# Optimization experiments

Measured on AMD Instinct MI355X. Metric: run time of the kernel, lower is better.

The kernel has to match this reference:

```python
import jax, jax.numpy as jnp
import numpy as np

N, M, DIST, HEADS, D, C, DFFN = 16384, 16, 2, 8, 256, 64, 512
DH = D // HEADS
GRID = 128
BLOCK = 2048  # mirrors torch batch_size loop in find_neighboring_voxels_optimized
EPS = 1e-5


def _neighbors(coords_f, src, m, dist):
    """Blockwise Manhattan-distance topk neighbor gather.
    coords_f: (N,3) float voxel coords; src: (N,D) features.
    Returns (N, m, D) neighbor features, zero-filled where fewer than m in range."""
    n = coords_f.shape[0]
    qblocks = coords_f.reshape(-1, BLOCK, 3)

    def one_block(cb):
        # (BLOCK, N) Manhattan distances
        d = jnp.abs(cb[:, None, :] - coords_f[None, :, :]).sum(-1)
        d = jnp.where(d <= dist, d, jnp.inf)
        vals, idx = jax.lax.top_k(-d, m)          # nearest m (self first: dist 0)
        valid = (vals > -jnp.inf)[..., None]
        return jnp.where(valid, src[idx], jnp.zeros((), src.dtype))

    return jax.lax.map(one_block, qblocks).reshape(n, m, src.shape[-1])


def _layernorm(x, g, b):
    mu = x.mean(-1, keepdims=True)
    var = ((x - mu) ** 2).mean(-1, keepdims=True)
    return (x - mu) * jax.lax.rsqrt(var + EPS) * g + b


def setup_inputs() -> dict:
    key = jax.random.key(0)
    ks = jax.random.split(key, 32)
    p = lambda i, shape, s: jax.random.normal(ks[i], shape, dtype=jnp.float32) * s
    z = lambda shape: jnp.zeros(shape, dtype=jnp.float32)
    o = lambda shape: jnp.ones(shape, dtype=jnp.float32)
    return {
        "coords": jax.random.randint(ks[0], (N, 3), 0, GRID, dtype=jnp.int32),
        "features": jax.random.normal(ks[1], (N, C), dtype=jnp.float32),
        "pe_w1": p(2, (3, D // 2), 0.5), "pe_b1": z((D // 2,)),
        "pe_w2": p(3, (D // 2, D), 0.08), "pe_b2": z((D,)),
        "proj_w": p(4, (C, D), 0.12), "proj_b": z((D,)),
        "wq": p(5, (D, D), 0.06), "bq": z((D,)),
        "wk": p(6, (D, D), 0.06), "bk": z((D,)),
        "wv": p(7, (D, D), 0.06), "bv": z((D,)),
        "wo": p(8, (D, D), 0.06), "bo": z((D,)),
        "ffn_w1": p(9, (D, DFFN), 0.06), "ffn_b1": z((DFFN,)),
        "ffn_w2": p(10, (DFFN, D), 0.04), "ffn_b2": z((D,)),
        "ln_g": o((D,)), "ln_b": z((D,)),
        "fus_w1": p(11, (D, C), 0.06), "fus_b1": z((C,)),
        "fus_w2": p(12, (2 * C, C), 0.09), "fus_b2": z((C,)),
        "bn_g": o((C,)), "bn_b": z((C,)),
    }


def reference(coords, features, pe_w1, pe_b1, pe_w2, pe_b2, proj_w, proj_b,
              wq, bq, wk, bk, wv, bv, wo, bo,
              ffn_w1, ffn_b1, ffn_w2, ffn_b2, ln_g, ln_b,
              fus_w1, fus_b1, fus_w2, fus_b2, bn_g, bn_b):
    coords_f = coords.astype(jnp.float32)
    # dynamic learnable positional encoding on normalized coords
    xn = coords_f / (GRID - 1)
    pe = jax.nn.relu(xn @ pe_w1 + pe_b1) @ pe_w2 + pe_b2
    src = features @ proj_w + proj_b + pe                       # (N, D)

    nf = _neighbors(coords_f, src, M, DIST)                     # (N, M, D)
    query = nf[:, 0, :]                                         # (N, D) self-feature

    # multihead attention: query len 1, key len M, batch N
    q = (query @ wq + bq).reshape(N, HEADS, DH)
    k = (nf @ wk + bk).reshape(N, M, HEADS, DH)
    v = (nf @ wv + bv).reshape(N, M, HEADS, DH)
    scores = jnp.einsum('nhd,nmhd->nhm', q, k) / jnp.sqrt(jnp.float32(DH))
    attn = jax.nn.softmax(scores, axis=-1)
    ao = jnp.einsum('nhm,nmhd->nhd', attn, v).reshape(N, D) @ wo + bo  # (N, D)

    # FFN with residual + LayerNorm (dropout=0 / eval)
    h = jax.nn.relu(ao @ ffn_w1 + ffn_b1) @ ffn_w2 + ffn_b2
    y = _layernorm(ao + h, ln_g, ln_b)                          # (N, D)

    # EnhancedFusion: project, concat, linear, BatchNorm1d (batch stats), ReLU
    t = y @ fus_w1 + fus_b1                                     # (N, C)
    f = jnp.concatenate([features, t], axis=1) @ fus_w2 + fus_b2
    mu = f.mean(0)
    var = ((f - mu) ** 2).mean(0)
    f = (f - mu) * jax.lax.rsqrt(var + EPS) * bn_g + bn_b
    return jax.nn.relu(f)                                       # (N, C)
```

## Files before the change

kernel.cpp:

```cpp
#include <hip/hip_runtime.h>
#include <stdint.h>

typedef unsigned short u16;
typedef unsigned int   u32;
typedef __attribute__((ext_vector_type(8))) short short8;
typedef __attribute__((ext_vector_type(4))) float f32x4;

static constexpr int kN = 16384;
static constexpr float kEPS = 1e-5f;

__device__ __forceinline__ u16 f2bf(float x) {
  u32 u = __float_as_uint(x);
  u32 r = (u + 0x7fffu + ((u >> 16) & 1u)) >> 16;
  return (u16)r;
}
__device__ __forceinline__ float bf2f(u16 x) {
  return __uint_as_float(((u32)x) << 16);
}
__device__ __forceinline__ void ldbf8(const u16* p, float* o) {
  uint4 v = *(const uint4*)p;
  o[0] = __uint_as_float(v.x << 16);  o[1] = __uint_as_float(v.x & 0xffff0000u);
  o[2] = __uint_as_float(v.y << 16);  o[3] = __uint_as_float(v.y & 0xffff0000u);
  o[4] = __uint_as_float(v.z << 16);  o[5] = __uint_as_float(v.z & 0xffff0000u);
  o[6] = __uint_as_float(v.w << 16);  o[7] = __uint_as_float(v.w & 0xffff0000u);
}
__device__ __forceinline__ void gll16(const u16* g, u16* l) {
  __builtin_amdgcn_global_load_lds(
      (const __attribute__((address_space(1))) void*)g,
      (__attribute__((address_space(3))) void*)l, 16, 0, 0);
}

struct WSet {
  const float* s[6]; u16* d[6];
  int K[6]; int N[6]; int dstride[6]; int coff[6];
};

__global__ __launch_bounds__(256) void k_setup(WSet ws,
                                               u32* __restrict__ zero_area,
                                               const float* __restrict__ proj_b,
                                               const float* __restrict__ pe_b2,
                                               const float* __restrict__ uw1,
                                               const float* __restrict__ ub1,
                                               const float* __restrict__ uw2,
                                               const float* __restrict__ ub2,
                                               u16* __restrict__ W2f,
                                               float* __restrict__ bbf,
                                               const int* __restrict__ coords,
                                               const float* __restrict__ feats,
                                               const float* __restrict__ pw1,
                                               const float* __restrict__ pb1,
                                               u16* __restrict__ A1,
                                               u16* __restrict__ A2,
                                               const float* __restrict__ wq,
                                               const float* __restrict__ wk,
                                               const float* __restrict__ wv,
                                               const float* __restrict__ proj_w_f,
                                               const float* __restrict__ pe_w2_f,
                                               u16* __restrict__ W1K,
                                               float* __restrict__ bcomb) {
  int w = blockIdx.y;
  if (w == 6) {
    int idx = blockIdx.x * 256 + threadIdx.x;
    if (idx < 33088) zero_area[idx] = 0u;
    return;
  }
  if (w == 7) {
    int n = blockIdx.x;
    if (n >= 64) return;
    int k = threadIdx.x;
    float s = 0.f;
    for (int j = 0; j < 64; j++) s += uw1[k * 64 + j] * uw2[(64 + j) * 64 + n];
    W2f[n * 320 + k] = f2bf(s);
    if (k < 64) W2f[n * 320 + 256 + k] = f2bf(uw2[k * 64 + n]);
    if (k == 0) {
      float b = ub2[n];
      for (int j = 0; j < 64; j++) b += ub1[j] * uw2[(64 + j) * 64 + n];
      bbf[n] = b;
    }
    return;
  }
  if (w == 8) {
    int r0 = blockIdx.x * 32;
#pragma unroll
    for (int s = 0; s < 3; s++) {
      int j = threadIdx.x + s * 256;
      int row = j / 24, seg = j % 24;
      int n = r0 + row;
      u16 o[8];
      if (seg < 8) {
        const float* fp = feats + (size_t)n * 64 + seg * 8;
        float4 a = *(const float4*)fp;
        float4 b = *(const float4*)(fp + 4);
        o[0] = f2bf(a.x); o[1] = f2bf(a.y); o[2] = f2bf(a.z); o[3] = f2bf(a.w);
        o[4] = f2bf(b.x); o[5] = f2bf(b.y); o[6] = f2bf(b.z); o[7] = f2bf(b.w);
        *(uint4*)(A2 + (size_t)n * 320 + 256 + seg * 8) = *(uint4*)o;
      } else {
        int jj0 = (seg - 8) * 8;
        float x0 = (float)coords[n * 3 + 0] * (1.f / 127.f);
        float x1 = (float)coords[n * 3 + 1] * (1.f / 127.f);
        float x2 = (float)coords[n * 3 + 2] * (1.f / 127.f);
#pragma unroll
        for (int u = 0; u < 8; u++) {
          int jj = jj0 + u;
          float hv = pb1[jj] + x0 * pw1[jj] + x1 * pw1[128 + jj] + x2 * pw1[256 + jj];
          o[u] = f2bf(fmaxf(hv, 0.f));
        }
      }
      *(uint4*)(A1 + (size_t)n * 192 + seg * 8) = *(uint4*)o;
    }
    return;
  }
  if (w == 9) {
    int bx = blockIdx.x;
    if (bx < 3) {
      const float* wsel = (bx == 0) ? wq : (bx == 1) ? wk : wv;
      int c = threadIdx.x;
      float s = 0.f;
      for (int d = 0; d < 256; d++) s += (proj_b[d] + pe_b2[d]) * wsel[d * 256 + c];
      bcomb[bx * 256 + c] = s;
    } else if (bx < 27) {
      int i0 = (bx - 3) * 2048 + threadIdx.x * 8;
      const float* src = (i0 < 16384) ? (proj_w_f + i0) : (pe_w2_f + (i0 - 16384));
      float4 a = *(const float4*)src;
      float4 b = *(const float4*)(src + 4);
      u16 o[8];
      o[0] = f2bf(a.x); o[1] = f2bf(a.y); o[2] = f2bf(a.z); o[3] = f2bf(a.w);
      o[4] = f2bf(b.x); o[5] = f2bf(b.y); o[6] = f2bf(b.z); o[7] = f2bf(b.w);
      *(uint4*)(W1K + i0) = *(uint4*)o;
    }
    return;
  }
  const float* S = ws.s[w]; u16* D = ws.d[w];
  int K = ws.K[w], N = ws.N[w], ds = ws.dstride[w], co = ws.coff[w];
  int ntx = N >> 5, tiles = ntx * (K >> 5);
  int t = blockIdx.x;
  if (t >= tiles) return;
  int n0 = (t % ntx) * 32, k0 = (t / ntx) * 32;
  __shared__ float st[32][33];
  int tr = threadIdx.x >> 3, tc4 = (threadIdx.x & 7) * 4;
  float4 v = *(const float4*)(S + (size_t)(k0 + tr) * N + n0 + tc4);
  st[tc4 + 0][tr] = v.x; st[tc4 + 1][tr] = v.y;
  st[tc4 + 2][tr] = v.z; st[tc4 + 3][tr] = v.w;
  __syncthreads();
  u16 o4[4];
  o4[0] = f2bf(st[tr][tc4 + 0]); o4[1] = f2bf(st[tr][tc4 + 1]);
  o4[2] = f2bf(st[tr][tc4 + 2]); o4[3] = f2bf(st[tr][tc4 + 3]);
  *(uint2*)(D + (size_t)(n0 + tr) * ds + co + k0 + tc4) = *(uint2*)o4;
}


__global__ __launch_bounds__(256) void k_hist(const int* __restrict__ coords,
                                              u32* __restrict__ cnt) {
  int n = blockIdx.x * 256 + threadIdx.x;
  int c = coords[n * 3] * 128 + coords[n * 3 + 1];
  atomicAdd(&cnt[c], 1u);
}

__global__ __launch_bounds__(256) void k_scan(const u32* __restrict__ cnt,
                                              u32* __restrict__ startb) {
  __shared__ u32 tots[256];
  int t = threadIdx.x;
  int base = t * 64;
  u32 s = 0;
  for (int i = 0; i < 64; i++) s += cnt[base + i];
  tots[t] = s;
  __syncthreads();
  if (t == 0) {
    u32 run = 0;
    for (int i = 0; i < 256; i++) { u32 v = tots[i]; tots[i] = run; run += v; }
  }
  __syncthreads();
  u32 run = tots[t];
  for (int i = 0; i < 64; i++) { startb[base + i] = run; run += cnt[base + i]; }
}

__global__ __launch_bounds__(256) void k_scatter(const int* __restrict__ coords,
                                                 const u32* __restrict__ startb,
                                                 u32* __restrict__ cursor,
                                                 u32* __restrict__ pts) {
  int n = blockIdx.x * 256 + threadIdx.x;
  int x = coords[n * 3], y = coords[n * 3 + 1], z = coords[n * 3 + 2];
  int c = x * 128 + y;
  u32 slot = atomicAdd(&cursor[c], 1u);
  pts[startb[c] + slot] = ((u32)z << 14) | (u32)n;
}

__global__ __launch_bounds__(256) void k_select(const int* __restrict__ coords,
                                                const u32* __restrict__ startb,
                                                const u32* __restrict__ cnt,
                                                const u32* __restrict__ pts,
                                                int* __restrict__ idxo) {
  int gid = blockIdx.x * 256 + threadIdx.x;
  u32 pk = pts[gid];
  int n = (int)(pk & 16383u);
  int z = (int)(pk >> 14);
  int x = coords[n * 3], y = coords[n * 3 + 1];
  u32 best[16];
#pragma unroll
  for (int j = 0; j < 16; j++) best[j] = 0xFFFFFFFFu;
  const int dxs[13] = {0, -1, 1, 0, 0, -2, 2, 0, 0, -1, -1, 1, 1};
  const int dys[13] = {0, 0, 0, -1, 1, 0, 0, -2, 2, -1, 1, -1, 1};
  const int dbs[13] = {0, 1, 1, 1, 1, 2, 2, 2, 2, 2, 2, 2, 2};
#pragma unroll
  for (int t = 0; t < 13; t++) {
    int xx = x + dxs[t], yy = y + dys[t];
    if (xx < 0 || xx > 127 || yy < 0 || yy > 127) continue;
    int c = xx * 128 + yy;
    u32 s0 = startb[c], e0 = s0 + cnt[c];
    for (u32 i = s0; i < e0; ++i) {
      u32 p = pts[i];
      int zq = (int)(p >> 14);
      int id = (int)(p & 16383u);
      int az = z - zq; az = az < 0 ? -az : az;
      int dd = dbs[t] + az;
      u32 key = (dd <= 2) ? (((u32)dd << 14) | (u32)id) : 0xFFFFFFFFu;
#pragma unroll
      for (int j = 0; j < 16; j++) {
        u32 lo = min(best[j], key);
        u32 hi = max(best[j], key);
        best[j] = lo; key = hi;
      }
    }
  }
#pragma unroll
  for (int j = 0; j < 16; j++)
    idxo[gid * 16 + j] = (best[j] == 0xFFFFFFFFu) ? -1 : (int)(best[j] & 16383u);
}

template <int BM, int BN, int ACT>
__global__ __launch_bounds__(256) void k_mgemm(
    const u16* __restrict__ A, const u16* __restrict__ WT,
    const float* __restrict__ bias,
    u16* __restrict__ Cout,
    int M, int K, int N) {
  constexpr int FM = BM / 32, FN = BN / 32;
  constexpr int RA = BM / 64, RB = BN / 64;
  constexpr int BNP = BN + 8;
  constexpr int STAGE = (BM + BN) * 128;
  constexpr int TILEB = BM * BNP * 2;
  constexpr int SMEMB = STAGE > TILEB ? STAGE : TILEB;
  __shared__ __align__(16) char smem[SMEMB];
  u16* AsB = (u16*)smem;
  u16* BsB = AsB + 2 * BM * 32;
  u16* tile = (u16*)smem;
  const int tid = threadIdx.x;
  const int wave = tid >> 6, lane = tid & 63;
  const int bm = blockIdx.y * BM, bn = blockIdx.x * BN;
  const int wr = (wave >> 1) * (BM / 2), wc = (wave & 1) * (BN / 2);
  const int fr = lane & 15, fk = (lane >> 4) * 8, rq = (lane >> 4) * 4;

  f32x4 acc[FM][FN];
#pragma unroll
  for (int i = 0; i < FM; i++)
#pragma unroll
    for (int j = 0; j < FN; j++)
#pragma unroll
      for (int r = 0; r < 4; r++) acc[i][j][r] = 0.f;

  for (int k0 = 0; k0 < K; k0 += 64) {
#pragma unroll
    for (int h = 0; h < 2; h++) {
#pragma unroll
      for (int r = 0; r < RA; r++) {
        int g2 = r * 256 + tid;
        gll16(A + (size_t)(bm + (g2 >> 2)) * K + k0 + h * 32 + (g2 & 3) * 8,
              AsB + h * BM * 32 + g2 * 8);
      }
#pragma unroll
      for (int r = 0; r < RB; r++) {
        int g2 = r * 256 + tid;
        gll16(WT + (size_t)(bn + (g2 >> 2)) * K + k0 + h * 32 + (g2 & 3) * 8,
              BsB + h * BN * 32 + g2 * 8);
      }
    }
    __syncthreads();
#pragma unroll
    for (int h = 0; h < 2; h++) {
      short8 af[FM], bg[FN];
#pragma unroll
      for (int i = 0; i < FM; i++)
        af[i] = *(const short8*)&AsB[h * BM * 32 + (wr + i * 16 + fr) * 32 + fk];
#pragma unroll
      for (int j = 0; j < FN; j++)
        bg[j] = *(const short8*)&BsB[h * BN * 32 + (wc + j * 16 + fr) * 32 + fk];
#pragma unroll
      for (int i = 0; i < FM; i++)
#pragma unroll
        for (int j = 0; j < FN; j++)
          acc[i][j] = __builtin_amdgcn_mfma_f32_16x16x32_bf16(af[i], bg[j], acc[i][j], 0, 0, 0);
    }
    __syncthreads();
  }

#pragma unroll
  for (int j = 0; j < FN; j++) {
    int ccl = wc + j * 16 + fr;
    float bval = bias ? bias[bn + ccl] : 0.f;
#pragma unroll
    for (int i = 0; i < FM; i++) {
      int rl = wr + i * 16 + rq;
#pragma unroll
      for (int r = 0; r < 4; r++) {
        float v = acc[i][j][r] + bval;
        if (ACT) v = fmaxf(v, 0.f);
        tile[(rl + r) * BNP + ccl] = f2bf(v);
      }
    }
  }
  __syncthreads();
  constexpr int RPW = BN / 8;
  constexpr int PT = BM * BN / 8 / 256;
#pragma unroll
  for (int t = 0; t < PT; t++) {
    int idx = t * 256 + tid;
    int row = idx / RPW, c8 = (idx % RPW) * 8;
    *(uint4*)(Cout + (size_t)(bm + row) * N + bn + c8) =
        *(const uint4*)&tile[row * BNP + c8];
  }
}

__global__ __launch_bounds__(256) void k_attn(const u16* __restrict__ QKV,
                                              const u32* __restrict__ pts,
                                              const int* __restrict__ idx,
                                              const float* __restrict__ bq,
                                              const float* __restrict__ bk,
                                              const float* __restrict__ bv,
                                              u16* __restrict__ outp) {
  int gid = blockIdx.x * 256 + threadIdx.x;
  int s4 = gid >> 3;
  int n = (int)(pts[s4] & 16383u), h = gid & 7;
  const int* ip = idx + s4 * 16;
  const int hb = h * 32;
  float q[32];
  {
    int i0 = ip[0];
    const u16* qp = QKV + (size_t)i0 * 768 + hb;
#pragma unroll
    for (int j = 0; j < 32; j += 8) ldbf8(qp + j, &q[j]);
#pragma unroll
    for (int j = 0; j < 32; j++) q[j] += bq[hb + j];
  }
  float qbk = 0.f;
#pragma unroll
  for (int j = 0; j < 32; j++) qbk += q[j] * bk[hb + j];
  float s[16]; int ii[16];
#pragma unroll
  for (int m = 0; m < 16; m++) {
    int i = ip[m]; ii[m] = i;
    float d = qbk;
    if (i >= 0) {
      const u16* kp = QKV + (size_t)i * 768 + 256 + hb;
      float kv[32];
#pragma unroll
      for (int j = 0; j < 32; j += 8) ldbf8(kp + j, &kv[j]);
#pragma unroll
      for (int j = 0; j < 32; j++) d += q[j] * kv[j];
    }
    s[m] = d * 0.17677669529663689f;
  }
  float mx = s[0];
#pragma unroll
  for (int m = 1; m < 16; m++) mx = fmaxf(mx, s[m]);
  float sum = 0.f;
#pragma unroll
  for (int m = 0; m < 16; m++) { s[m] = __expf(s[m] - mx); sum += s[m]; }
  float inv = 1.f / sum;
  float o[32];
#pragma unroll
  for (int j = 0; j < 32; j++) o[j] = 0.f;
#pragma unroll
  for (int m = 0; m < 16; m++) {
    if (ii[m] >= 0) {
      const u16* vp = QKV + (size_t)ii[m] * 768 + 512 + hb;
      float vv[32];
#pragma unroll
      for (int j = 0; j < 32; j += 8) ldbf8(vp + j, &vv[j]);
#pragma unroll
      for (int j = 0; j < 32; j++) o[j] += s[m] * vv[j];
    }
  }
  u16* op = outp + (size_t)n * 256 + hb;
#pragma unroll
  for (int j = 0; j < 32; j += 8) {
    u16 tmp[8];
#pragma unroll
    for (int jj = 0; jj < 8; jj++) tmp[jj] = f2bf(o[j + jj] * inv + bv[hb + j + jj]);
    *(uint4*)(op + j) = *(uint4*)tmp;
  }
}

__global__ __launch_bounds__(256) void k_ffn2ln(const u16* __restrict__ A,
                                                const u16* __restrict__ WT,
                                                const float* __restrict__ bias,
                                                const u16* __restrict__ Addp,
                                                const float* __restrict__ g,
                                                const float* __restrict__ b,
                                                u16* __restrict__ A2) {
  constexpr int BM = 64, BN = 256, FM = 2, FN = 8;
  constexpr int ADP = 264;
  __shared__ __align__(16) char smem[(BM + BN) * 128];
  __shared__ float lnS[64][2], lnQ[64][2];
  u16* AsB = (u16*)smem;
  u16* BsB = AsB + 2 * BM * 32;
  u16* addT = (u16*)smem;
  u16* outT = (u16*)smem;
  const int tid = threadIdx.x;
  const int wave = tid >> 6, lane = tid & 63;
  const int bm = blockIdx.x * BM;
  const int wr = (wave >> 1) * 32, wc = (wave & 1) * 128;
  const int fr = lane & 15, fk = (lane >> 4) * 8, rq = (lane >> 4) * 4;

  f32x4 acc[FM][FN];
#pragma unroll
  for (int i = 0; i < FM; i++)
#pragma unroll
    for (int j = 0; j < FN; j++)
#pragma unroll
      for (int r = 0; r < 4; r++) acc[i][j][r] = 0.f;

  for (int k0 = 0; k0 < 512; k0 += 64) {
#pragma unroll
    for (int h = 0; h < 2; h++) {
      {
        int g2 = tid;
        gll16(A + (size_t)(bm + (g2 >> 2)) * 512 + k0 + h * 32 + (g2 & 3) * 8,
              AsB + h * BM * 32 + g2 * 8);
      }
#pragma unroll
      for (int r = 0; r < 4; r++) {
        int g2 = r * 256 + tid;
        gll16(WT + (size_t)(g2 >> 2) * 512 + k0 + h * 32 + (g2 & 3) * 8,
              BsB + h * BN * 32 + g2 * 8);
      }
    }
    __syncthreads();
#pragma unroll
    for (int h = 0; h < 2; h++) {
      short8 af[FM], bg[FN];
#pragma unroll
      for (int i = 0; i < FM; i++)
        af[i] = *(const short8*)&AsB[h * BM * 32 + (wr + i * 16 + fr) * 32 + fk];
#pragma unroll
      for (int j = 0; j < FN; j++)
        bg[j] = *(const short8*)&BsB[h * BN * 32 + (wc + j * 16 + fr) * 32 + fk];
#pragma unroll
      for (int i = 0; i < FM; i++)
#pragma unroll
        for (int j = 0; j < FN; j++)
          acc[i][j] = __builtin_amdgcn_mfma_f32_16x16x32_bf16(af[i], bg[j], acc[i][j], 0, 0, 0);
    }
    __syncthreads();
  }

#pragma unroll
  for (int t = 0; t < 8; t++) {
    int idx = t * 256 + tid;
    int row = idx >> 5, c8 = (idx & 31) * 8;
    *(uint4*)&addT[row * ADP + c8] =
        *(const uint4*)(Addp + (size_t)(bm + row) * 256 + c8);
  }
  __syncthreads();
#pragma unroll
  for (int j = 0; j < FN; j++) {
    int cc = wc + j * 16 + fr;
    float bval = bias[cc];
#pragma unroll
    for (int i = 0; i < FM; i++) {
      int rl = wr + i * 16 + rq;
#pragma unroll
      for (int r = 0; r < 4; r++)
        acc[i][j][r] += bval + bf2f(addT[(rl + r) * ADP + cc]);
    }
  }
#pragma unroll
  for (int i = 0; i < FM; i++) {
#pragma unroll
    for (int r = 0; r < 4; r++) {
      float sm = 0.f, sq = 0.f;
#pragma unroll
      for (int j = 0; j < FN; j++) { float t = acc[i][j][r]; sm += t; sq += t * t; }
#pragma unroll
      for (int off = 1; off < 16; off <<= 1) {
        sm += __shfl_xor(sm, off);
        sq += __shfl_xor(sq, off);
      }
      if (fr == 0) {
        int row = wr + i * 16 + rq + r;
        lnS[row][wave & 1] = sm;
        lnQ[row][wave & 1] = sq;
      }
    }
  }
  __syncthreads();
#pragma unroll
  for (int i = 0; i < FM; i++) {
#pragma unroll
    for (int r = 0; r < 4; r++) {
      int row = wr + i * 16 + rq + r;
      float sm = lnS[row][0] + lnS[row][1];
      float sq = lnQ[row][0] + lnQ[row][1];
      float mu = sm * (1.f / 256.f);
      float var = sq * (1.f / 256.f) - mu * mu;
      float rstd = rsqrtf(var + kEPS);
#pragma unroll
      for (int j = 0; j < FN; j++) {
        int cc = wc + j * 16 + fr;
        float val = (acc[i][j][r] - mu) * rstd * g[cc] + b[cc];
        outT[row * ADP + cc] = f2bf(val);
      }
    }
  }
  __syncthreads();
#pragma unroll
  for (int t = 0; t < 8; t++) {
    int idx = t * 256 + tid;
    int row = idx >> 5, c8 = (idx & 31) * 8;
    *(uint4*)(A2 + (size_t)(bm + row) * 320 + c8) =
        *(const uint4*)&outT[row * ADP + c8];
  }
}

__global__ __launch_bounds__(256) void k_fgemm(const u16* __restrict__ A2,
                                               const u16* __restrict__ W2f,
                                               const float* __restrict__ bbf,
                                               float* __restrict__ fB,
                                               float* __restrict__ pS,
                                               float* __restrict__ pQ) {
  __shared__ __align__(16) u16 As[2][2048];
  __shared__ __align__(16) u16 Bs[2][2048];
  __shared__ float colS[64][2], colQ[64][2];
  const int tid = threadIdx.x;
  const int wave = tid >> 6, lane = tid & 63;
  const int bm = blockIdx.x * 64;
  const int wr = (wave >> 1) * 32, wc = (wave & 1) * 32;
  const int fr = lane & 15, fk = (lane >> 4) * 8, rq = (lane >> 4) * 4;
  const int g = wave * 64 + lane;
  const int grow = g >> 2, gko = (g & 3) * 8;

  f32x4 acc[2][2];
#pragma unroll
  for (int i = 0; i < 2; i++)
#pragma unroll
    for (int j = 0; j < 2; j++)
#pragma unroll
      for (int r = 0; r < 4; r++) acc[i][j][r] = 0.f;
  for (int k0 = 0; k0 < 320; k0 += 64) {
#pragma unroll
    for (int h = 0; h < 2; h++) {
      gll16(A2 + (size_t)(bm + grow) * 320 + k0 + h * 32 + gko, As[h] + g * 8);
      gll16(W2f + (size_t)grow * 320 + k0 + h * 32 + gko, Bs[h] + g * 8);
    }
    __syncthreads();
#pragma unroll
    for (int h = 0; h < 2; h++) {
      short8 af[2], bg[2];
#pragma unroll
      for (int i = 0; i < 2; i++)
        af[i] = *(const short8*)&As[h][(wr + i * 16 + fr) * 32 + fk];
#pragma unroll
      for (int j = 0; j < 2; j++)
        bg[j] = *(const short8*)&Bs[h][(wc + j * 16 + fr) * 32 + fk];
#pragma unroll
      for (int i = 0; i < 2; i++)
#pragma unroll
        for (int j = 0; j < 2; j++)
          acc[i][j] = __builtin_amdgcn_mfma_f32_16x16x32_bf16(af[i], bg[j], acc[i][j], 0, 0, 0);
    }
    __syncthreads();
  }
  float cS[2] = {0.f, 0.f}, cQ[2] = {0.f, 0.f};
#pragma unroll
  for (int j = 0; j < 2; j++) {
    int col = wc + j * 16 + fr;
    float bv = bbf[col];
#pragma unroll
    for (int i = 0; i < 2; i++) {
      int rbase = bm + wr + i * 16 + rq;
#pragma unroll
      for (int r = 0; r < 4; r++) {
        float v = acc[i][j][r] + bv;
        fB[(size_t)(rbase + r) * 64 + col] = v;
        cS[j] += v; cQ[j] += v * v;
      }
    }
  }
#pragma unroll
  for (int off = 16; off < 64; off <<= 1) {
#pragma unroll
    for (int j = 0; j < 2; j++) {
      cS[j] += __shfl_xor(cS[j], off);
      cQ[j] += __shfl_xor(cQ[j], off);
    }
  }
  if ((lane >> 4) == 0) {
#pragma unroll
    for (int j = 0; j < 2; j++) {
      colS[wc + j * 16 + fr][wave >> 1] = cS[j];
      colQ[wc + j * 16 + fr][wave >> 1] = cQ[j];
    }
  }
  __syncthreads();
  if (tid < 64) {
    atomicAdd(&pS[tid], colS[tid][0] + colS[tid][1]);
    atomicAdd(&pQ[tid], colQ[tid][0] + colQ[tid][1]);
  }
}

__global__ __launch_bounds__(256) void k_bnapply(const float* __restrict__ f,
                                                 const float* __restrict__ pS,
                                                 const float* __restrict__ pQ,
                                                 const float* __restrict__ g,
                                                 const float* __restrict__ b,
                                                 float* __restrict__ out) {
  __shared__ float cf_s[64], sh_s[64];
  if (threadIdx.x < 64) {
    int c = threadIdx.x;
    float S = pS[c], Q = pQ[c];
    float m = S * (1.f / 16384.f);
    float var = Q * (1.f / 16384.f) - m * m;
    float cf = rsqrtf(var + kEPS) * g[c];
    cf_s[c] = cf;
    sh_s[c] = b[c] - m * cf;
  }
  __syncthreads();
  int gid = blockIdx.x * 256 + threadIdx.x;
  int e = gid * 4, col = e & 63;
  float4 v = *(const float4*)(f + e);
  float4 cf = *(const float4*)(cf_s + col);
  float4 sh = *(const float4*)(sh_s + col);
  float4 o;
  o.x = fmaxf(v.x * cf.x + sh.x, 0.f);
  o.y = fmaxf(v.y * cf.y + sh.y, 0.f);
  o.z = fmaxf(v.z * cf.z + sh.z, 0.f);
  o.w = fmaxf(v.w * cf.w + sh.w, 0.f);
  *(float4*)(out + e) = o;
}

extern "C" void kernel_launch(void* const* d_in, const int* in_sizes, int n_in,
                              void* d_out, int out_size, void* d_ws, size_t ws_size,
                              hipStream_t stream) {
  (void)in_sizes; (void)n_in; (void)out_size; (void)ws_size;
  const int*   coords = (const int*)d_in[0];
  const float* feats  = (const float*)d_in[1];
  const float* pe_w1  = (const float*)d_in[2];
  const float* pe_b1  = (const float*)d_in[3];
  const float* pe_w2  = (const float*)d_in[4];
  const float* pe_b2  = (const float*)d_in[5];
  const float* proj_w = (const float*)d_in[6];
  const float* proj_b = (const float*)d_in[7];
  const float* wq  = (const float*)d_in[8];
  const float* bq  = (const float*)d_in[9];
  const float* wk  = (const float*)d_in[10];
  const float* bk  = (const float*)d_in[11];
  const float* wv  = (const float*)d_in[12];
  const float* bv  = (const float*)d_in[13];
  const float* wo  = (const float*)d_in[14];
  const float* bo  = (const float*)d_in[15];
  const float* fw1 = (const float*)d_in[16];
  const float* fb1 = (const float*)d_in[17];
  const float* fw2 = (const float*)d_in[18];
  const float* fb2 = (const float*)d_in[19];
  const float* lng = (const float*)d_in[20];
  const float* lnb = (const float*)d_in[21];
  const float* uw1 = (const float*)d_in[22];
  const float* ub1 = (const float*)d_in[23];
  const float* uw2 = (const float*)d_in[24];
  const float* ub2 = (const float*)d_in[25];
  const float* bng = (const float*)d_in[26];
  const float* bnb = (const float*)d_in[27];
  float* out = (float*)d_out;

  char* Wc = (char*)d_ws;
  const size_t MB = 1u << 20;
  u16*   A1    = (u16*)(Wc + 0 * MB);
  u16*   QKVb  = (u16*)(Wc + 14 * MB);
  u16*   aoInB = (u16*)(Wc + 38 * MB);
  u16*   aoB   = (u16*)(Wc + 46 * MB);
  u16*   h1B   = (u16*)(Wc + 54 * MB);
  u16*   A2    = (u16*)(Wc + 78 * MB);
  float* fB    = (float*)(Wc + 0 * MB);

  u16* qkvT  = (u16*)(Wc + 88 * MB);
  u16* woT   = qkvT + 196608;
  u16* fw1T  = woT + 65536;
  u16* fw2T  = fw1T + 131072;
  u16* W1K   = fw2T + 131072;
  u16* W2f   = W1K + 49152;
  u16* Wcomb = W2f + 20480;
  float* bbf   = (float*)(Wcomb + 147456);
  float* bcomb = bbf + 64;

  u32* Z      = (u32*)(Wc + 90 * MB);
  u32* cnt    = Z;
  u32* cursor = Z + 16384;
  float* pS   = (float*)(Z + 32768);
  float* pQ   = (float*)(Z + 32832);
  u32* startb = Z + 33280;
  u32* pts    = Z + 49664;
  int* idxb   = (int*)(Z + 66048);

  WSet ws;
  ws.s[0] = wq;     ws.d[0] = qkvT;          ws.K[0] = 256; ws.N[0] = 256; ws.dstride[0] = 256; ws.coff[0] = 0;
  ws.s[1] = wk;     ws.d[1] = qkvT + 65536;  ws.K[1] = 256; ws.N[1] = 256; ws.dstride[1] = 256; ws.coff[1] = 0;
  ws.s[2] = wv;     ws.d[2] = qkvT + 131072; ws.K[2] = 256; ws.N[2] = 256; ws.dstride[2] = 256; ws.coff[2] = 0;
  ws.s[3] = wo;     ws.d[3] = woT;           ws.K[3] = 256; ws.N[3] = 256; ws.dstride[3] = 256; ws.coff[3] = 0;
  ws.s[4] = fw1;    ws.d[4] = fw1T;          ws.K[4] = 256; ws.N[4] = 512; ws.dstride[4] = 256; ws.coff[4] = 0;
  ws.s[5] = fw2;    ws.d[5] = fw2T;          ws.K[5] = 512; ws.N[5] = 256; ws.dstride[5] = 512; ws.coff[5] = 0;

  k_setup<<<dim3(512, 10), 256, 0, stream>>>(ws, Z, proj_b, pe_b2,
                                             uw1, ub1, uw2, ub2, W2f, bbf,
                                             coords, feats, pe_w1, pe_b1, A1, A2,
                                             wq, wk, wv, proj_w, pe_w2, W1K, bcomb);
  k_mgemm<64, 64, 0><<<dim3(3, 12), 256, 0, stream>>>(
      qkvT, W1K, nullptr, Wcomb, 768, 256, 192);
  k_hist<<<64, 256, 0, stream>>>(coords, cnt);
  k_scan<<<1, 256, 0, stream>>>(cnt, startb);
  k_scatter<<<64, 256, 0, stream>>>(coords, startb, cursor, pts);
  k_select<<<64, 256, 0, stream>>>(coords, startb, cnt, pts, idxb);
  k_mgemm<128, 128, 0><<<dim3(6, 128), 256, 0, stream>>>(
      A1, Wcomb, bcomb, QKVb, kN, 192, 768);
  k_attn<<<512, 256, 0, stream>>>(QKVb, pts, idxb, bq, bk, bv, aoInB);
  k_mgemm<128, 64, 0><<<dim3(4, 128), 256, 0, stream>>>(
      aoInB, woT, bo, aoB, kN, 256, 256);
  k_mgemm<128, 128, 1><<<dim3(4, 128), 256, 0, stream>>>(
      aoB, fw1T, fb1, h1B, kN, 256, 512);
  k_ffn2ln<<<256, 256, 0, stream>>>(h1B, fw2T, fb2, aoB, lng, lnb, A2);
  k_fgemm<<<256, 256, 0, stream>>>(A2, W2f, bbf, fB, pS, pQ);
  k_bnapply<<<1024, 256, 0, stream>>>(fB, pS, pQ, bng, bnb, out);
}
```

Before: 242.9 us.

## Fold output projection into FFN weights and merge weight-prep with histogram

Removes the separate attention output projection GEMM. Wo is folded algebraically into FFN W1 (Wcomb2 = Wo·W1, with a combined bias). The residual ao + h is computed inside the final GEMM by concatenating the attention input and h1 along K (768) against a stacked [Wo; W2] weight, so the ao tensor is never written or re-read. The small weight-combining GEMMs and the coordinate histogram are merged into one launch, and the scan now uses wave shuffles. The combined weights add extra bf16 rounding, and the last GEMM does more K work per tile.

```diff
diff --git a/kernel.cpp b/kernel.cpp
--- a/kernel.cpp
+++ b/kernel.cpp
@@ -57,7 +57,13 @@
                                                const float* __restrict__ proj_w_f,
                                                const float* __restrict__ pe_w2_f,
                                                u16* __restrict__ W1K,
-                                               float* __restrict__ bcomb) {
+                                               float* __restrict__ bcomb,
+                                               const float* __restrict__ wo_f,
+                                               const float* __restrict__ fw1_f,
+                                               const float* __restrict__ bo_f,
+                                               const float* __restrict__ fb1_f,
+                                               u16* __restrict__ woK,
+                                               float* __restrict__ bcomb2) {
   int w = blockIdx.y;
   if (w == 6) {
     int idx = blockIdx.x * 256 + threadIdx.x;
@@ -127,6 +133,19 @@
       o[0] = f2bf(a.x); o[1] = f2bf(a.y); o[2] = f2bf(a.z); o[3] = f2bf(a.w);
       o[4] = f2bf(b.x); o[5] = f2bf(b.y); o[6] = f2bf(b.z); o[7] = f2bf(b.w);
       *(uint4*)(W1K + i0) = *(uint4*)o;
+    } else if (bx < 59) {
+      int i0 = (bx - 27) * 2048 + threadIdx.x * 8;
+      float4 a = *(const float4*)(wo_f + i0);
+      float4 b = *(const float4*)(wo_f + i0 + 4);
+      u16 o[8];
+      o[0] = f2bf(a.x); o[1] = f2bf(a.y); o[2] = f2bf(a.z); o[3] = f2bf(a.w);
+      o[4] = f2bf(b.x); o[5] = f2bf(b.y); o[6] = f2bf(b.z); o[7] = f2bf(b.w);
+      *(uint4*)(woK + i0) = *(uint4*)o;
+    } else if (bx < 61) {
+      int n2 = (bx - 59) * 256 + threadIdx.x;
+      float s = fb1_f[n2];
+      for (int d = 0; d < 256; d++) s += bo_f[d] * fw1_f[d * 512 + n2];
+      bcomb2[n2] = s;
     }
     return;
   }
@@ -148,29 +167,111 @@
   *(uint2*)(D + (size_t)(n0 + tr) * ds + co + k0 + tc4) = *(uint2*)o4;
 }
 
-
-__global__ __launch_bounds__(256) void k_hist(const int* __restrict__ coords,
-                                              u32* __restrict__ cnt) {
-  int n = blockIdx.x * 256 + threadIdx.x;
-  int c = coords[n * 3] * 128 + coords[n * 3 + 1];
-  atomicAdd(&cnt[c], 1u);
-}
+__global__ __launch_bounds__(256) void k_combo(const u16* __restrict__ qkvT,
+                                               const u16* __restrict__ W1K,
+                                               u16* __restrict__ Wcomb,
+                                               const u16* __restrict__ fw1T,
+                                               const u16* __restrict__ woK,
+                                               u16* __restrict__ Wcomb2,
+                                               const int* __restrict__ coords,
+                                               u32* __restrict__ cnt) {
+  int y = blockIdx.y;
+  if (y >= 20) {
+    int n = ((y - 20) * 4 + blockIdx.x) * 256 + threadIdx.x;
+    int c = coords[n * 3] * 128 + coords[n * 3 + 1];
+    atomicAdd(&cnt[c], 1u);
+    return;
+  }
+  const u16 *A, *WT; u16* C; int K, N, bm, bn;
+  if (y < 12) {
+    if (blockIdx.x >= 3) return;
+    A = qkvT; WT = W1K; C = Wcomb; K = 256; N = 192;
+    bm = y * 64; bn = blockIdx.x * 64;
+  } else {
+    A = fw1T; WT = woK; C = Wcomb2; K = 256; N = 256;
+    bm = (y - 12) * 64; bn = blockIdx.x * 64;
+  }
+  __shared__ __align__(16) char smem[16384];
+  u16* AsB = (u16*)smem;
+  u16* BsB = AsB + 2 * 64 * 32;
+  u16* tile = (u16*)smem;
+  const int tid = threadIdx.x;
+  const int wave = tid >> 6, lane = tid & 63;
+  const int wr = (wave >> 1) * 32, wc = (wave & 1) * 32;
+  const int fr = lane & 15, fk = (lane >> 4) * 8, rq = (lane >> 4) * 4;
+  const int grow = tid >> 2, gko = (tid & 3) * 8;
+
+  f32x4 acc[2][2];
+#pragma unroll
+  for (int i = 0; i < 2; i++)
+#pragma unroll
+    for (int j = 0; j < 2; j++)
+#pragma unroll
+      for (int r = 0; r < 4; r++) acc[i][j][r] = 0.f;
+
+  for (int k0 = 0; k0 < K; k0 += 64) {
+#pragma unroll
+    for (int h = 0; h < 2; h++) {
+      gll16(A + (size_t)(bm + grow) * K + k0 + h * 32 + gko, AsB + h * 2048 + tid * 8);
+      gll16(WT + (size_t)(bn + grow) * K + k0 + h * 32 + gko, BsB + h * 2048 + tid * 8);
+    }
+    __syncthreads();
+#pragma unroll
+    for (int h = 0; h < 2; h++) {
+      short8 af[2], bg[2];
+#pragma unroll
+      for (int i = 0; i < 2; i++)
+        af[i] = *(const short8*)&AsB[h * 2048 + (wr + i * 16 + fr) * 32 + fk];
+#pragma unroll
+      for (int j = 0; j < 2; j++)
+        bg[j] = *(const short8*)&BsB[h * 2048 + (wc + j * 16 + fr) * 32 + fk];
+#pragma unroll
+      for (int i = 0; i < 2; i++)
+#pragma unroll
+        for (int j = 0; j < 2; j++)
+          acc[i][j] = __builtin_amdgcn_mfma_f32_16x16x32_bf16(af[i], bg[j], acc[i][j], 0, 0, 0);
+    }
+    __syncthreads();
+  }
+#pragma unroll
+  for (int j = 0; j < 2; j++) {
+    int ccl = wc + j * 16 + fr;
+#pragma unroll
+    for (int i = 0; i < 2; i++) {
+      int rl = wr + i * 16 + rq;
+#pragma unroll
+      for (int r = 0; r < 4; r++) tile[(rl + r) * 72 + ccl] = f2bf(acc[i][j][r]);
+    }
+  }
+  __syncthreads();
+#pragma unroll
+  for (int t = 0; t < 2; t++) {
+    int idx = t * 256 + tid;
+    int row = idx >> 3, c8 = (idx & 7) * 8;
+    *(uint4*)(C + (size_t)(bm + row) * N + bn + c8) = *(const uint4*)&tile[row * 72 + c8];
+  }
+}
+
 
 __global__ __launch_bounds__(256) void k_scan(const u32* __restrict__ cnt,
                                               u32* __restrict__ startb) {
-  __shared__ u32 tots[256];
+  __shared__ u32 wsum[4];
   int t = threadIdx.x;
+  int lane = t & 63, wid = t >> 6;
   int base = t * 64;
   u32 s = 0;
   for (int i = 0; i < 64; i++) s += cnt[base + i];
-  tots[t] = s;
+  u32 v = s;
+#pragma unroll
+  for (int off = 1; off < 64; off <<= 1) {
+    u32 u = __shfl_up(v, off);
+    if (lane >= off) v += u;
+  }
+  if (lane == 63) wsum[wid] = v;
   __syncthreads();
-  if (t == 0) {
-    u32 run = 0;
-    for (int i = 0; i < 256; i++) { u32 v = tots[i]; tots[i] = run; run += v; }
-  }
-  __syncthreads();
-  u32 run = tots[t];
+  u32 woff = 0;
+  for (int w2 = 0; w2 < wid; w2++) woff += wsum[w2];
+  u32 run = woff + v - s;
   for (int i = 0; i < 64; i++) { startb[base + i] = run; run += cnt[base + i]; }
 }
 
@@ -232,7 +333,7 @@
     const u16* __restrict__ A, const u16* __restrict__ WT,
     const float* __restrict__ bias,
     u16* __restrict__ Cout,
-    int M, int K, int N) {
+    int M, int K, int N, int lda, int ldc) {
   constexpr int FM = BM / 32, FN = BN / 32;
   constexpr int RA = BM / 64, RB = BN / 64;
   constexpr int BNP = BN + 8;
@@ -263,7 +364,7 @@
 #pragma unroll
       for (int r = 0; r < RA; r++) {
         int g2 = r * 256 + tid;
-        gll16(A + (size_t)(bm + (g2 >> 2)) * K + k0 + h * 32 + (g2 & 3) * 8,
+        gll16(A + (size_t)(bm + (g2 >> 2)) * lda + k0 + h * 32 + (g2 & 3) * 8,
               AsB + h * BM * 32 + g2 * 8);
       }
 #pragma unroll
@@ -314,7 +415,7 @@
   for (int t = 0; t < PT; t++) {
     int idx = t * 256 + tid;
     int row = idx / RPW, c8 = (idx % RPW) * 8;
-    *(uint4*)(Cout + (size_t)(bm + row) * N + bn + c8) =
+    *(uint4*)(Cout + (size_t)(bm + row) * ldc + bn + c8) =
         *(const uint4*)&tile[row * BNP + c8];
   }
 }
@@ -379,7 +480,7 @@
       for (int j = 0; j < 32; j++) o[j] += s[m] * vv[j];
     }
   }
-  u16* op = outp + (size_t)n * 256 + hb;
+  u16* op = outp + (size_t)n * 768 + hb;
 #pragma unroll
   for (int j = 0; j < 32; j += 8) {
     u16 tmp[8];
@@ -389,10 +490,10 @@
   }
 }
 
-__global__ __launch_bounds__(256) void k_ffn2ln(const u16* __restrict__ A,
-                                                const u16* __restrict__ WT,
-                                                const float* __restrict__ bias,
-                                                const u16* __restrict__ Addp,
+__global__ __launch_bounds__(256) void k_ffn2ln(const u16* __restrict__ AH,
+                                                const u16* __restrict__ WTBIG,
+                                                const float* __restrict__ bo,
+                                                const float* __restrict__ fb2,
                                                 const float* __restrict__ g,
                                                 const float* __restrict__ b,
                                                 u16* __restrict__ A2) {
@@ -402,7 +503,6 @@
   __shared__ float lnS[64][2], lnQ[64][2];
   u16* AsB = (u16*)smem;
   u16* BsB = AsB + 2 * BM * 32;
-  u16* addT = (u16*)smem;
   u16* outT = (u16*)smem;
   const int tid = threadIdx.x;
   const int wave = tid >> 6, lane = tid & 63;
@@ -418,18 +518,18 @@
 #pragma unroll
       for (int r = 0; r < 4; r++) acc[i][j][r] = 0.f;
 
-  for (int k0 = 0; k0 < 512; k0 += 64) {
+  for (int k0 = 0; k0 < 768; k0 += 64) {
 #pragma unroll
     for (int h = 0; h < 2; h++) {
       {
         int g2 = tid;
-        gll16(A + (size_t)(bm + (g2 >> 2)) * 512 + k0 + h * 32 + (g2 & 3) * 8,
+        gll16(AH + (size_t)(bm + (g2 >> 2)) * 768 + k0 + h * 32 + (g2 & 3) * 8,
               AsB + h * BM * 32 + g2 * 8);
       }
 #pragma unroll
       for (int r = 0; r < 4; r++) {
         int g2 = r * 256 + tid;
-        gll16(WT + (size_t)(g2 >> 2) * 512 + k0 + h * 32 + (g2 & 3) * 8,
+        gll16(WTBIG + (size_t)(g2 >> 2) * 768 + k0 + h * 32 + (g2 & 3) * 8,
               BsB + h * BN * 32 + g2 * 8);
       }
     }
@@ -453,24 +553,13 @@
   }
 
 #pragma unroll
-  for (int t = 0; t < 8; t++) {
-    int idx = t * 256 + tid;
-    int row = idx >> 5, c8 = (idx & 31) * 8;
-    *(uint4*)&addT[row * ADP + c8] =
-        *(const uint4*)(Addp + (size_t)(bm + row) * 256 + c8);
-  }
-  __syncthreads();
-#pragma unroll
   for (int j = 0; j < FN; j++) {
     int cc = wc + j * 16 + fr;
-    float bval = bias[cc];
-#pragma unroll
-    for (int i = 0; i < FM; i++) {
-      int rl = wr + i * 16 + rq;
-#pragma unroll
-      for (int r = 0; r < 4; r++)
-        acc[i][j][r] += bval + bf2f(addT[(rl + r) * ADP + cc]);
-    }
+    float bval = bo[cc] + fb2[cc];
+#pragma unroll
+    for (int i = 0; i < FM; i++)
+#pragma unroll
+      for (int r = 0; r < 4; r++) acc[i][j][r] += bval;
   }
 #pragma unroll
   for (int i = 0; i < FM; i++) {
@@ -674,21 +763,21 @@
   const size_t MB = 1u << 20;
   u16*   A1    = (u16*)(Wc + 0 * MB);
   u16*   QKVb  = (u16*)(Wc + 14 * MB);
-  u16*   aoInB = (u16*)(Wc + 38 * MB);
-  u16*   aoB   = (u16*)(Wc + 46 * MB);
-  u16*   h1B   = (u16*)(Wc + 54 * MB);
+  u16*   AH    = (u16*)(Wc + 38 * MB);
   u16*   A2    = (u16*)(Wc + 78 * MB);
   float* fB    = (float*)(Wc + 0 * MB);
 
-  u16* qkvT  = (u16*)(Wc + 88 * MB);
-  u16* woT   = qkvT + 196608;
-  u16* fw1T  = woT + 65536;
-  u16* fw2T  = fw1T + 131072;
-  u16* W1K   = fw2T + 131072;
-  u16* W2f   = W1K + 49152;
-  u16* Wcomb = W2f + 20480;
-  float* bbf   = (float*)(Wcomb + 147456);
-  float* bcomb = bbf + 64;
+  u16* qkvT   = (u16*)(Wc + 88 * MB);
+  u16* WTBIG  = qkvT + 196608;
+  u16* fw1T   = WTBIG + 196608;
+  u16* woK    = fw1T + 131072;
+  u16* W1K    = woK + 65536;
+  u16* W2f    = W1K + 49152;
+  u16* Wcomb  = W2f + 20480;
+  u16* Wcomb2 = Wcomb + 147456;
+  float* bbf    = (float*)(Wcomb2 + 131072);
+  float* bcomb  = bbf + 64;
+  float* bcomb2 = bcomb + 768;
 
   u32* Z      = (u32*)(Wc + 90 * MB);
   u32* cnt    = Z;
@@ -700,31 +789,29 @@
   int* idxb   = (int*)(Z + 66048);
 
   WSet ws;
-  ws.s[0] = wq;     ws.d[0] = qkvT;          ws.K[0] = 256; ws.N[0] = 256; ws.dstride[0] = 256; ws.coff[0] = 0;
-  ws.s[1] = wk;     ws.d[1] = qkvT + 65536;  ws.K[1] = 256; ws.N[1] = 256; ws.dstride[1] = 256; ws.coff[1] = 0;
-  ws.s[2] = wv;     ws.d[2] = qkvT + 131072; ws.K[2] = 256; ws.N[2] = 256; ws.dstride[2] = 256; ws.coff[2] = 0;
-  ws.s[3] = wo;     ws.d[3] = woT;           ws.K[3] = 256; ws.N[3] = 256; ws.dstride[3] = 256; ws.coff[3] = 0;
-  ws.s[4] = fw1;    ws.d[4] = fw1T;          ws.K[4] = 256; ws.N[4] = 512; ws.dstride[4] = 256; ws.coff[4] = 0;
-  ws.s[5] = fw2;    ws.d[5] = fw2T;          ws.K[5] = 512; ws.N[5] = 256; ws.dstride[5] = 512; ws.coff[5] = 0;
+  ws.s[0] = wq;  ws.d[0] = qkvT;          ws.K[0] = 256; ws.N[0] = 256; ws.dstride[0] = 256; ws.coff[0] = 0;
+  ws.s[1] = wk;  ws.d[1] = qkvT + 65536;  ws.K[1] = 256; ws.N[1] = 256; ws.dstride[1] = 256; ws.coff[1] = 0;
+  ws.s[2] = wv;  ws.d[2] = qkvT + 131072; ws.K[2] = 256; ws.N[2] = 256; ws.dstride[2] = 256; ws.coff[2] = 0;
+  ws.s[3] = wo;  ws.d[3] = WTBIG;         ws.K[3] = 256; ws.N[3] = 256; ws.dstride[3] = 768; ws.coff[3] = 0;
+  ws.s[4] = fw1; ws.d[4] = fw1T;          ws.K[4] = 256; ws.N[4] = 512; ws.dstride[4] = 256; ws.coff[4] = 0;
+  ws.s[5] = fw2; ws.d[5] = WTBIG;         ws.K[5] = 512; ws.N[5] = 256; ws.dstride[5] = 768; ws.coff[5] = 256;
 
   k_setup<<<dim3(512, 10), 256, 0, stream>>>(ws, Z, proj_b, pe_b2,
                                              uw1, ub1, uw2, ub2, W2f, bbf,
                                              coords, feats, pe_w1, pe_b1, A1, A2,
-                                             wq, wk, wv, proj_w, pe_w2, W1K, bcomb);
-  k_mgemm<64, 64, 0><<<dim3(3, 12), 256, 0, stream>>>(
-      qkvT, W1K, nullptr, Wcomb, 768, 256, 192);
-  k_hist<<<64, 256, 0, stream>>>(coords, cnt);
+                                             wq, wk, wv, proj_w, pe_w2, W1K, bcomb,
+                                             wo, fw1, bo, fb1, woK, bcomb2);
+  k_combo<<<dim3(4, 36), 256, 0, stream>>>(qkvT, W1K, Wcomb, fw1T, woK, Wcomb2,
+                                           coords, cnt);
   k_scan<<<1, 256, 0, stream>>>(cnt, startb);
   k_scatter<<<64, 256, 0, stream>>>(coords, startb, cursor, pts);
   k_select<<<64, 256, 0, stream>>>(coords, startb, cnt, pts, idxb);
   k_mgemm<128, 128, 0><<<dim3(6, 128), 256, 0, stream>>>(
-      A1, Wcomb, bcomb, QKVb, kN, 192, 768);
-  k_attn<<<512, 256, 0, stream>>>(QKVb, pts, idxb, bq, bk, bv, aoInB);
-  k_mgemm<128, 64, 0><<<dim3(4, 128), 256, 0, stream>>>(
-      aoInB, woT, bo, aoB, kN, 256, 256);
+      A1, Wcomb, bcomb, QKVb, kN, 192, 768, 192, 768);
+  k_attn<<<512, 256, 0, stream>>>(QKVb, pts, idxb, bq, bk, bv, AH);
   k_mgemm<128, 128, 1><<<dim3(4, 128), 256, 0, stream>>>(
-      aoB, fw1T, fb1, h1B, kN, 256, 512);
-  k_ffn2ln<<<256, 256, 0, stream>>>(h1B, fw2T, fb2, aoB, lng, lnb, A2);
+      AH, Wcomb2, bcomb2, AH + 256, kN, 256, 512, 768, 768);
+  k_ffn2ln<<<256, 256, 0, stream>>>(AH, WTBIG, bo, fb2, lng, lnb, A2);
   k_fgemm<<<256, 256, 0, stream>>>(A2, W2f, bbf, fB, pS, pQ);
   k_bnapply<<<1024, 256, 0, stream>>>(fB, pS, pQ, bng, bnb, out);
 }
```

Result: faster. 236.2 us (-2.8%).
